# Optimization experiments

Hardware: AMD Instinct MI355X
Metric: run time of the kernel (lower is better)

Reference implementation:

```python
import jax, jax.numpy as jnp
import numpy as np
from jax import lax

P = 0.1  # WTA keep fraction (mode='per_image')


def setup_inputs() -> dict:
    key = jax.random.key(0)
    x = jax.random.normal(key, (32, 256, 64, 64), dtype=jnp.float32)
    return {"x": x}


def reference(x) -> jnp.ndarray:
    bs, nc, sz, _ = x.shape
    k = int(np.ceil(nc * sz * sz * P))  # 104858 for these shapes
    flat = x.reshape(bs, -1)                      # [bs, nc*sz*sz]
    topk_vals = lax.top_k(flat, k)[0]             # [bs, k], descending
    thr = topk_vals[:, -1].reshape(bs, 1, 1, 1)   # k-th largest per image
    return x * (x >= thr).astype(x.dtype)
```

## Files before the change

kernel.cpp:

```cpp
#include <hip/hip_runtime.h>
#include <hip/hip_bf16.h>
#include <stdint.h>


#define IMGS    32
#define NPER    1048576
#define NPER4   (NPER / 4)
#define NBINS   8192
#define BPI_H   32
#define BPI_M   64
#define CAP     16384
#define LCAP    2048
#define CSTRIDE 64

typedef float floatx4 __attribute__((ext_vector_type(4)));

__device__ __forceinline__ unsigned mapf(float f) {
    unsigned u = __float_as_uint(f);
    return (u & 0x80000000u) ? ~u : (u | 0x80000000u);
}

__device__ __forceinline__ void block_scan256(unsigned* p, int t, unsigned v) {
    p[t] = v;
    __syncthreads();
    #pragma unroll
    for (int off = 1; off < 256; off <<= 1) {
        unsigned u = (t >= off) ? p[t - off] : 0u;
        __syncthreads();
        p[t] += u;
        __syncthreads();
    }
}

__global__ void k_zero(uint4* __restrict__ p, int n16) {
    int i = blockIdx.x * blockDim.x + threadIdx.x;
    if (i < n16) p[i] = make_uint4(0u, 0u, 0u, 0u);
}

__global__ void k_hist(const float4* __restrict__ x4, unsigned* __restrict__ hist) {
    __shared__ unsigned h[NBINS];
    int t = threadIdx.x;
    for (int j = t; j < NBINS; j += 256) h[j] = 0u;
    __syncthreads();

    int bx = blockIdx.x;
    int img = bx >> 5;
    long long base4 = (long long)img * NPER4 + (long long)(bx & 31) * 8192;
    float4 v0 = x4[base4 + t];
    for (int it = 0; it < 31; ++it) {
        float4 v1 = x4[base4 + (it + 1) * 256 + t];
        atomicAdd(&h[mapf(v0.x) >> 19], 1u);
        atomicAdd(&h[mapf(v0.y) >> 19], 1u);
        atomicAdd(&h[mapf(v0.z) >> 19], 1u);
        atomicAdd(&h[mapf(v0.w) >> 19], 1u);
        v0 = v1;
    }
    atomicAdd(&h[mapf(v0.x) >> 19], 1u);
    atomicAdd(&h[mapf(v0.y) >> 19], 1u);
    atomicAdd(&h[mapf(v0.z) >> 19], 1u);
    atomicAdd(&h[mapf(v0.w) >> 19], 1u);
    __syncthreads();

    unsigned* gh = hist + (long long)img * NBINS;
    for (int j = t; j < NBINS; j += 256) {
        unsigned c = h[j];
        if (c) atomicAdd(&gh[j], c);
    }
}

__global__ void k_scan(const unsigned* __restrict__ hist, uint2* __restrict__ binfo,
                       unsigned k) {
    int img = blockIdx.x;
    const unsigned* h = hist + (long long)img * NBINS;
    __shared__ unsigned bins[NBINS];
    __shared__ unsigned pre[256];
    int t = threadIdx.x;

    for (int idx = t; idx < NBINS; idx += 256) bins[idx] = h[idx];
    __syncthreads();

    unsigned s = 0;
    #pragma unroll
    for (int j = 0; j < 32; ++j) s += bins[t * 32 + ((j + t) & 31)];

    block_scan256(pre, t, s);
    unsigned total_above = pre[255] - pre[t];
    if (total_above < k && total_above + s >= k) {
        unsigned cum = total_above;
        for (int j = 31; j >= 0; --j) {
            unsigned v = bins[t * 32 + j];
            cum += v;
            if (cum >= k) {
                binfo[img] = make_uint2((unsigned)(t * 32 + j), k - (cum - v));
                break;
            }
        }
    }
}

__global__ void k_mask(const float4* __restrict__ x4, float4* __restrict__ o4,
                       const uint2* __restrict__ binfo, unsigned* __restrict__ counters,
                       unsigned* __restrict__ candKey, unsigned* __restrict__ candIdx) {
    __shared__ unsigned lkey[LCAP];
    __shared__ unsigned lidx[LCAP];
    __shared__ unsigned lcnt;
    __shared__ unsigned gbase;
    int t = threadIdx.x;
    if (t == 0) lcnt = 0u;
    __syncthreads();

    int bx = blockIdx.x;
    int img = bx >> 6;
    unsigned b13 = binfo[img].x;
    long long base4 = (long long)img * NPER4 + (long long)(bx & 63) * 4096;

    for (int it = 0; it < 16; ++it) {
        long long i = base4 + it * 256 + t;
        float4 v = x4[i];
        unsigned ebase = (unsigned)(i & (NPER4 - 1)) * 4u;
        float4 o;
        float* vp = &v.x;
        float* op = &o.x;
        #pragma unroll
        for (int j = 0; j < 4; ++j) {
            float c = vp[j];
            unsigned key = mapf(c);
            unsigned t13 = key >> 19;
            op[j] = (t13 >= b13) ? c : 0.0f;
            if (t13 == b13) {
                unsigned p = atomicAdd(&lcnt, 1u);
                if (p < LCAP) { lkey[p] = key; lidx[p] = ebase + (unsigned)j; }
            }
        }
        floatx4 ov = { o.x, o.y, o.z, o.w };
        __builtin_nontemporal_store(ov, (floatx4*)&o4[i]);
    }
    __syncthreads();

    unsigned n = lcnt;
    if (n > LCAP) n = LCAP;
    if (t == 0) gbase = atomicAdd(&counters[img * CSTRIDE], n);
    __syncthreads();
    unsigned gb = gbase;
    long long cb = (long long)img * CAP;
    for (unsigned j = t; j < n; j += 256u) {
        unsigned pos = gb + j;
        if (pos < CAP) {
            candKey[cb + pos] = lkey[j];
            candIdx[cb + pos] = lidx[j];
        }
    }
}

__global__ void k_select_fix(float* __restrict__ out,
                             const uint2* __restrict__ binfo,
                             const unsigned* __restrict__ counters,
                             const unsigned* __restrict__ candKey,
                             const unsigned* __restrict__ candIdx) {
    int img = blockIdx.x;
    __shared__ unsigned klds[CAP];
    __shared__ unsigned h2[2048];
    __shared__ unsigned h256[256];
    __shared__ unsigned pre[256];
    __shared__ unsigned sh_p11, sh_r2, sh_thr;
    int t = threadIdx.x;

    unsigned cnt = counters[img * CSTRIDE];
    if (cnt > CAP) cnt = CAP;
    unsigned r = binfo[img].y;
    const unsigned* ck = candKey + (long long)img * CAP;
    const unsigned* ci = candIdx + (long long)img * CAP;

    for (int j = t; j < 2048; j += 256) h2[j] = 0u;
    __syncthreads();

    for (unsigned j = t; j < cnt; j += 256u) {
        unsigned kl = ck[j] & 0x7FFFFu;
        klds[j] = kl;
        atomicAdd(&h2[kl >> 8], 1u);
    }
    __syncthreads();

    unsigned s = 0;
    #pragma unroll
    for (int j = 0; j < 8; ++j) s += h2[t * 8 + ((j + t) & 7)];
    block_scan256(pre, t, s);
    unsigned above = pre[255] - pre[t];
    if (above < r && above + s >= r) {
        unsigned cum = above;
        for (int j = 7; j >= 0; --j) {
            unsigned v = h2[t * 8 + j];
            cum += v;
            if (cum >= r) {
                sh_p11 = (unsigned)(t * 8 + j);
                sh_r2 = r - (cum - v);
                break;
            }
        }
    }
    __syncthreads();
    unsigned p11 = sh_p11, r2 = sh_r2;

    h256[t] = 0u;
    __syncthreads();
    for (unsigned j = t; j < cnt; j += 256u) {
        unsigned kl = klds[j];
        if ((kl >> 8) == p11) atomicAdd(&h256[kl & 0xFFu], 1u);
    }
    __syncthreads();
    unsigned v = h256[t];
    block_scan256(pre, t, v);
    unsigned above2 = pre[255] - pre[t];
    if (above2 < r2 && above2 + v >= r2)
        sh_thr = (p11 << 8) | (unsigned)t;
    __syncthreads();
    unsigned thr = sh_thr;

    float* oi = out + (long long)img * NPER;
    for (unsigned j = t; j < cnt; j += 256u) {
        if (klds[j] < thr) oi[ci[j]] = 0.0f;
    }
}

extern "C" void kernel_launch(void* const* d_in, const int* in_sizes, int n_in,
                              void* d_out, int out_size, void* d_ws, size_t ws_size,
                              hipStream_t stream) {
    const float* x = (const float*)d_in[0];
    float* out = (float*)d_out;
    unsigned k = (unsigned)((NPER + 9) / 10);

    char* ws = (char*)d_ws;
    size_t histB = (size_t)IMGS * NBINS * 4;
    size_t cntB  = (size_t)IMGS * CSTRIDE * 4;
    unsigned* hist     = (unsigned*)ws;
    unsigned* counters = (unsigned*)(ws + histB);
    uint2*    binfo    = (uint2*)   (ws + histB + cntB);
    unsigned* candKey  = (unsigned*)(ws + histB + cntB + 1024);
    unsigned* candIdx  = (unsigned*)(ws + histB + cntB + 1024
                                        + (size_t)IMGS * CAP * 4);

    int n16 = (int)((histB + cntB) / 16);
    k_zero<<<dim3((n16 + 255) / 256), dim3(256), 0, stream>>>((uint4*)ws, n16);

    dim3 blk(256);
    k_hist<<<dim3(IMGS * BPI_H), blk, 0, stream>>>((const float4*)x, hist);
    k_scan<<<dim3(IMGS), blk, 0, stream>>>(hist, binfo, k);
    k_mask<<<dim3(IMGS * BPI_M), blk, 0, stream>>>((const float4*)x, (float4*)out,
                                                   binfo, counters, candKey, candIdx);
    k_select_fix<<<dim3(IMGS), blk, 0, stream>>>(out, binfo, counters, candKey, candIdx);
}
```

Before: 114.0 us.

## Pack histogram into 16-bit LDS counters and fuse threshold scan into mask kernel

The histogram kernel now packs two 16-bit bin counters per LDS word, which halves its shared memory use, and it runs twice as many blocks, each covering a smaller slice. The separate k_scan kernel is removed. Every k_mask block now scans its image's global histogram itself to find the threshold bin, and one block per image writes binfo for the later fixup kernel. This drops one launch and raises occupancy in the histogram pass, at the cost of 64 blocks per image each re-reading the 8192-bin histogram from global memory.

After: 121.4 us. 6.5% more time.

```diff
diff --git a/kernel.cpp b/kernel.cpp
--- a/kernel.cpp
+++ b/kernel.cpp
@@ -7,7 +7,8 @@
 #define NPER    1048576
 #define NPER4   (NPER / 4)
 #define NBINS   8192
-#define BPI_H   32
+#define HWORDS  4096
+#define BPI_H   64
 #define BPI_M   64
 #define CAP     16384
 #define LCAP    2048
@@ -38,82 +39,80 @@
 }
 
 __global__ void k_hist(const float4* __restrict__ x4, unsigned* __restrict__ hist) {
-    __shared__ unsigned h[NBINS];
+    __shared__ unsigned h[HWORDS];
     int t = threadIdx.x;
-    for (int j = t; j < NBINS; j += 256) h[j] = 0u;
+    for (int j = t; j < HWORDS; j += 256) h[j] = 0u;
     __syncthreads();
 
     int bx = blockIdx.x;
-    int img = bx >> 5;
-    long long base4 = (long long)img * NPER4 + (long long)(bx & 31) * 8192;
+    int img = bx >> 6;
+    long long base4 = (long long)img * NPER4 + (long long)(bx & 63) * 4096;
     float4 v0 = x4[base4 + t];
-    for (int it = 0; it < 31; ++it) {
+    for (int it = 0; it < 15; ++it) {
         float4 v1 = x4[base4 + (it + 1) * 256 + t];
-        atomicAdd(&h[mapf(v0.x) >> 19], 1u);
-        atomicAdd(&h[mapf(v0.y) >> 19], 1u);
-        atomicAdd(&h[mapf(v0.z) >> 19], 1u);
-        atomicAdd(&h[mapf(v0.w) >> 19], 1u);
+        unsigned b;
+        b = mapf(v0.x) >> 19; atomicAdd(&h[b >> 1], 1u << ((b & 1) << 4));
+        b = mapf(v0.y) >> 19; atomicAdd(&h[b >> 1], 1u << ((b & 1) << 4));
+        b = mapf(v0.z) >> 19; atomicAdd(&h[b >> 1], 1u << ((b & 1) << 4));
+        b = mapf(v0.w) >> 19; atomicAdd(&h[b >> 1], 1u << ((b & 1) << 4));
         v0 = v1;
     }
-    atomicAdd(&h[mapf(v0.x) >> 19], 1u);
-    atomicAdd(&h[mapf(v0.y) >> 19], 1u);
-    atomicAdd(&h[mapf(v0.z) >> 19], 1u);
-    atomicAdd(&h[mapf(v0.w) >> 19], 1u);
+    {
+        unsigned b;
+        b = mapf(v0.x) >> 19; atomicAdd(&h[b >> 1], 1u << ((b & 1) << 4));
+        b = mapf(v0.y) >> 19; atomicAdd(&h[b >> 1], 1u << ((b & 1) << 4));
+        b = mapf(v0.z) >> 19; atomicAdd(&h[b >> 1], 1u << ((b & 1) << 4));
+        b = mapf(v0.w) >> 19; atomicAdd(&h[b >> 1], 1u << ((b & 1) << 4));
+    }
     __syncthreads();
 
     unsigned* gh = hist + (long long)img * NBINS;
-    for (int j = t; j < NBINS; j += 256) {
-        unsigned c = h[j];
-        if (c) atomicAdd(&gh[j], c);
-    }
-}
-
-__global__ void k_scan(const unsigned* __restrict__ hist, uint2* __restrict__ binfo,
+    for (int w = t; w < HWORDS; w += 256) {
+        unsigned v = h[w];
+        unsigned c0 = v & 0xFFFFu, c1 = v >> 16;
+        if (c0) atomicAdd(&gh[2 * w], c0);
+        if (c1) atomicAdd(&gh[2 * w + 1], c1);
+    }
+}
+
+__global__ void k_mask(const float4* __restrict__ x4, float4* __restrict__ o4,
+                       const unsigned* __restrict__ hist, uint2* __restrict__ binfo,
+                       unsigned* __restrict__ counters,
+                       unsigned* __restrict__ candKey, unsigned* __restrict__ candIdx,
                        unsigned k) {
-    int img = blockIdx.x;
-    const unsigned* h = hist + (long long)img * NBINS;
-    __shared__ unsigned bins[NBINS];
+    __shared__ unsigned lkey[LCAP];
+    __shared__ unsigned lidx[LCAP];
     __shared__ unsigned pre[256];
+    __shared__ unsigned lcnt, gbase, sb13, sr;
     int t = threadIdx.x;
 
-    for (int idx = t; idx < NBINS; idx += 256) bins[idx] = h[idx];
-    __syncthreads();
+    int bx = blockIdx.x;
+    int img = bx >> 6;
+    const unsigned* gh = hist + (long long)img * NBINS;
 
     unsigned s = 0;
     #pragma unroll
-    for (int j = 0; j < 32; ++j) s += bins[t * 32 + ((j + t) & 31)];
-
+    for (int j = 0; j < 32; ++j) s += gh[t * 32 + j];
     block_scan256(pre, t, s);
-    unsigned total_above = pre[255] - pre[t];
-    if (total_above < k && total_above + s >= k) {
-        unsigned cum = total_above;
+    unsigned above = pre[255] - pre[t];
+    if (above < k && above + s >= k) {
+        unsigned cum = above;
         for (int j = 31; j >= 0; --j) {
-            unsigned v = bins[t * 32 + j];
+            unsigned v = gh[t * 32 + j];
             cum += v;
             if (cum >= k) {
-                binfo[img] = make_uint2((unsigned)(t * 32 + j), k - (cum - v));
+                sb13 = (unsigned)(t * 32 + j);
+                sr = k - (cum - v);
                 break;
             }
         }
     }
-}
-
-__global__ void k_mask(const float4* __restrict__ x4, float4* __restrict__ o4,
-                       const uint2* __restrict__ binfo, unsigned* __restrict__ counters,
-                       unsigned* __restrict__ candKey, unsigned* __restrict__ candIdx) {
-    __shared__ unsigned lkey[LCAP];
-    __shared__ unsigned lidx[LCAP];
-    __shared__ unsigned lcnt;
-    __shared__ unsigned gbase;
-    int t = threadIdx.x;
     if (t == 0) lcnt = 0u;
     __syncthreads();
-
-    int bx = blockIdx.x;
-    int img = bx >> 6;
-    unsigned b13 = binfo[img].x;
+    unsigned b13 = sb13;
+    if ((bx & 63) == 0 && t == 0) binfo[img] = make_uint2(sb13, sr);
+
     long long base4 = (long long)img * NPER4 + (long long)(bx & 63) * 4096;
-
     for (int it = 0; it < 16; ++it) {
         long long i = base4 + it * 256 + t;
         float4 v = x4[i];
@@ -244,8 +243,8 @@
 
     dim3 blk(256);
     k_hist<<<dim3(IMGS * BPI_H), blk, 0, stream>>>((const float4*)x, hist);
-    k_scan<<<dim3(IMGS), blk, 0, stream>>>(hist, binfo, k);
     k_mask<<<dim3(IMGS * BPI_M), blk, 0, stream>>>((const float4*)x, (float4*)out,
-                                                   binfo, counters, candKey, candIdx);
+                                                   hist, binfo, counters,
+                                                   candKey, candIdx, k);
     k_select_fix<<<dim3(IMGS), blk, 0, stream>>>(out, binfo, counters, candKey, candIdx);
 }
```
